# Kernel tuning notes

Hardware: AMD Instinct MI355X
Metric: run time of the kernel (lower is better)

Reference implementation:

```python
import jax, jax.numpy as jnp
import numpy as np

B, N, VD, QD, D, H, NG, P = 512, 36, 2048, 1024, 1024, 16, 20, 64
DH = D // H  # per-head dim = 64


def setup_inputs() -> dict:
    key = jax.random.key(0)
    ks = jax.random.split(key, 20)
    s = 0.02
    return {
        "visual": jax.random.normal(ks[0], (B, N, VD), jnp.float32),
        "pos_emb": jax.random.uniform(ks[1], (B, N, NG, P), jnp.float32),
        "question": jax.random.normal(ks[2], (B, QD), jnp.float32),
        # v2out: FC v_dim -> out_dim with ReLU
        "v2out_w": s * jax.random.normal(ks[3], (VD, D), jnp.float32),
        "v2out_b": jnp.zeros((D,), jnp.float32),
        # GAttNet self_weights: (out_dim+q_dim) -> out_dim, no activation
        "self_w": s * jax.random.normal(ks[4], (D + QD, D), jnp.float32),
        "self_b": jnp.zeros((D,), jnp.float32),
        # attention query/key projections (feat_dim -> feat_dim)
        "q_w": s * jax.random.normal(ks[5], (D, D), jnp.float32),
        "q_b": jnp.zeros((D,), jnp.float32),
        "k_w": s * jax.random.normal(ks[6], (D, D), jnp.float32),
        "k_b": jnp.zeros((D,), jnp.float32),
        # pair_pos_fc1: pos_emb_dim -> num_heads (fc_dim)
        "pos_w": s * jax.random.normal(ks[7], (P, H), jnp.float32),
        "pos_b": jnp.zeros((H,), jnp.float32),
        # label bias FC: label_num(=1) -> 1, with bias (label_bias=True)
        "bias_w": s * jax.random.normal(ks[8], (1, 1), jnp.float32),
        "bias_b": jnp.zeros((1,), jnp.float32),
        # grouped 1x1 conv linear_out_: per-head [feat_dim -> feat_dim/H]
        "out_w": s * jax.random.normal(ks[9], (H, D, DH), jnp.float32),
        "out_b": jnp.zeros((D,), jnp.float32),
    }


def reference(visual, pos_emb, question, v2out_w, v2out_b, self_w, self_b,
              q_w, q_b, k_w, k_b, pos_w, pos_b, bias_w, bias_b, out_w, out_b):
    b, n, _ = visual.shape
    ng = pos_emb.shape[2]

    # v2out projection (FCNet default ReLU)
    vis = jax.nn.relu(visual @ v2out_w + v2out_b)  # [B,N,D]

    # dense all-ones adjacency [B,N,N,1]; condensed over labels and sliced to nongt
    adj = jnp.ones((b, n, ng), vis.dtype)                       # sum over label dim
    label_bias = adj * bias_w[0, 0] + bias_b[0]                  # [B,N,NG]

    # --- single propagation step (num_steps=1) ---
    # concat_visual_question with mask
    row_mask = (jnp.sum(vis, axis=-1) != 0).astype(vis.dtype)    # [B,N]
    q_bcast = question[:, None, :] * row_mask[..., None]         # [B,N,QD]
    v_cat_q = jnp.concatenate([vis, q_bcast], axis=-1)           # [B,N,D+QD]

    # GAttNet: self loop features
    self_feat = v_cat_q @ self_w + self_b                        # [B,N,D]

    # GraphSelfAttentionLayer on self_feat
    ngf = self_feat[:, :ng]                                      # [B,NG,D]
    q = (self_feat @ q_w + q_b).reshape(b, n, H, DH)             # [B,N,H,DH]
    k = (ngf @ k_w + k_b).reshape(b, ng, H, DH)                  # [B,NG,H,DH]
    scale = np.float32(1.0 / np.sqrt(DH))
    aff = jnp.einsum('bnhd,bmhd->bnhm', q, k) * scale            # [B,N,H,NG]

    # relational position bias: relu -> clamp -> log
    pos_feat = jax.nn.relu(pos_emb @ pos_w + pos_b)              # [B,N,NG,H]
    aff = aff + jnp.transpose(jnp.log(jnp.maximum(pos_feat, 1e-6)), (0, 1, 3, 2))

    # adjacency mask + label bias
    aff = jnp.where(adj[:, :, None, :] > 0, aff, jnp.float32(-9e15))
    aff = aff + label_bias[:, :, None, :]

    attn = jax.nn.softmax(aff, axis=-1)                          # [B,N,H,NG]
    out_t = jnp.einsum('bnhm,bmf->bnhf', attn, ngf)              # [B,N,H,D]
    neighbor = jnp.einsum('bnhf,hfd->bnhd', out_t, out_w).reshape(b, n, D) + out_b

    imp_rel = jax.nn.relu(self_feat + neighbor)                  # GAttNet output

    # residual connection
    return vis + imp_rel
```

## Files before the change

### kernel.cpp

```cpp
#include <hip/hip_runtime.h>
#include <cstdint>

#define AS1 __attribute__((address_space(1)))
#define AS3 __attribute__((address_space(3)))

typedef __bf16 bf16x8 __attribute__((ext_vector_type(8)));
typedef float f32x4 __attribute__((ext_vector_type(4)));

__device__ __forceinline__ unsigned short f2bf(float f) {
  unsigned u = __float_as_uint(f);
  u += 0x7FFFu + ((u >> 16) & 1u);
  return (unsigned short)(u >> 16);
}
__device__ __forceinline__ float bf2f(unsigned short s) {
  return __uint_as_float(((unsigned)s) << 16);
}

__global__ void k_f32_to_bf16(const float* __restrict__ in,
                              unsigned short* __restrict__ out, long n8) {
  long i = (long)blockIdx.x * blockDim.x + threadIdx.x;
  if (i >= n8) return;
  const float4* p = (const float4*)in + i * 2;
  float4 a = p[0], b = p[1];
  uint4 o;
  o.x = (unsigned)f2bf(a.x) | ((unsigned)f2bf(a.y) << 16);
  o.y = (unsigned)f2bf(a.z) | ((unsigned)f2bf(a.w) << 16);
  o.z = (unsigned)f2bf(b.x) | ((unsigned)f2bf(b.y) << 16);
  o.w = (unsigned)f2bf(b.z) | ((unsigned)f2bf(b.w) << 16);
  *((uint4*)out + i) = o;
}

__global__ void k_transpose_bf16(const float* __restrict__ in,
                                 unsigned short* __restrict__ out, int R, int C) {
  __shared__ float tile[32][33];
  int c0 = blockIdx.x * 32, r0 = blockIdx.y * 32;
  int tx = threadIdx.x & 31, ty = threadIdx.x >> 5;
  #pragma unroll
  for (int i = ty; i < 32; i += 8) tile[i][tx] = in[(long)(r0 + i) * C + c0 + tx];
  __syncthreads();
  #pragma unroll
  for (int i = ty; i < 32; i += 8) out[(long)(c0 + i) * R + r0 + tx] = f2bf(tile[tx][i]);
}

__global__ void k_transpose_outw(const float* __restrict__ in,
                                 unsigned short* __restrict__ out) {
  __shared__ float tile[32][33];
  int d0 = blockIdx.x * 32, f0 = blockIdx.y * 32, h = blockIdx.z;
  int tx = threadIdx.x & 31, ty = threadIdx.x >> 5;
  #pragma unroll
  for (int i = ty; i < 32; i += 8)
    tile[i][tx] = in[((long)h * 1024 + f0 + i) * 64 + d0 + tx];
  __syncthreads();
  #pragma unroll
  for (int i = ty; i < 32; i += 8)
    out[((long)h * 64 + d0 + i) * 1024 + f0 + tx] = f2bf(tile[tx][i]);
}

enum { EPI_VIS = 0, EPI_QW, EPI_SELF, EPI_Q, EPI_K, EPI_KG };

template <int EPI>
__global__ __launch_bounds__(256) void k_gemm(
    const unsigned short* __restrict__ A, const unsigned short* __restrict__ Bt,
    int M, int K,
    const float* __restrict__ bias,
    const float* __restrict__ mask, const float* __restrict__ QW,
    float* __restrict__ outf, unsigned short* __restrict__ outb,
    unsigned short* __restrict__ ngf) {
  (void)M;
  __shared__ __align__(16) unsigned short As[128 * 64];
  __shared__ __align__(16) unsigned short Bs[128 * 64];
  const int t = threadIdx.x;
  const int l = t & 63, w = t >> 6;
  const int wm = w >> 1, wn = w & 1;
  const long bm0 = (long)blockIdx.y * 128, bn0 = (long)blockIdx.x * 128;

  f32x4 acc[4][4];
  #pragma unroll
  for (int i = 0; i < 4; ++i)
    #pragma unroll
    for (int j = 0; j < 4; ++j) acc[i][j] = (f32x4){0.f, 0.f, 0.f, 0.f};

  const int lrow = l & 15;
  const int lkbase = (l >> 4) * 8;

  for (int k0 = 0; k0 < K; k0 += 64) {
    #pragma unroll
    for (int i = 0; i < 4; ++i) {
      int c = i * 256 + t;
      int row = c >> 3, cc = (c & 7) << 3;
      const unsigned short* ga = A + (bm0 + row) * (long)K + k0 + cc;
      const unsigned short* gb = Bt + (bn0 + row) * (long)K + k0 + cc;
      int ldsoff = __builtin_amdgcn_readfirstlane((i * 256 + w * 64) * 8);
      __builtin_amdgcn_global_load_lds((AS1 void*)ga, (AS3 void*)(As + ldsoff), 16, 0, 0);
      __builtin_amdgcn_global_load_lds((AS1 void*)gb, (AS3 void*)(Bs + ldsoff), 16, 0, 0);
    }
    __syncthreads();
    #pragma unroll
    for (int kk = 0; kk < 2; ++kk) {
      bf16x8 af[4], bfr[4];
      const int lk = kk * 32 + lkbase;
      #pragma unroll
      for (int mf = 0; mf < 4; ++mf)
        af[mf] = *(const bf16x8*)(As + (wm * 64 + mf * 16 + lrow) * 64 + lk);
      #pragma unroll
      for (int nf = 0; nf < 4; ++nf)
        bfr[nf] = *(const bf16x8*)(Bs + (wn * 64 + nf * 16 + lrow) * 64 + lk);
      #pragma unroll
      for (int mf = 0; mf < 4; ++mf)
        #pragma unroll
        for (int nf = 0; nf < 4; ++nf)
          acc[mf][nf] = __builtin_amdgcn_mfma_f32_16x16x32_bf16(af[mf], bfr[nf],
                                                                acc[mf][nf], 0, 0, 0);
    }
    __syncthreads();
  }

  #pragma unroll
  for (int mf = 0; mf < 4; ++mf) {
    #pragma unroll
    for (int r = 0; r < 4; ++r) {
      long row = bm0 + wm * 64 + mf * 16 + ((l >> 4) << 2) + r;
      #pragma unroll
      for (int nf = 0; nf < 4; ++nf) {
        long col = bn0 + wn * 64 + nf * 16 + (l & 15);
        float x = acc[mf][nf][r];
        long idx = row * 1024 + col;
        if (EPI == EPI_VIS) {
          x += bias[col];
          x = fmaxf(x, 0.f);
          outf[idx] = x;
          outb[idx] = f2bf(x);
        } else if (EPI == EPI_QW) {
          outf[idx] = x;
        } else if (EPI == EPI_SELF) {
          int b = (int)(row / 36), n = (int)(row % 36);
          x += bias[col] + mask[row] * QW[(long)b * 1024 + col];
          outf[idx] = x;
          outb[idx] = f2bf(x);
          if (n < 20) ngf[((long)b * 20 + n) * 1024 + col] = f2bf(x);
        } else if (EPI == EPI_Q) {
          x += bias[col];
          outb[idx] = f2bf(x);
        } else if (EPI == EPI_K) {
          x += bias[col];
          outb[idx] = f2bf(x);
        } else {
          outb[idx] = f2bf(x);
        }
      }
    }
  }
}

__global__ void k_mask(const float* __restrict__ vis, float* __restrict__ mask) {
  int row = blockIdx.x * 4 + (threadIdx.x >> 6);
  int l = threadIdx.x & 63;
  const float4* vr = (const float4*)(vis + (long)row * 1024);
  float s = 0.f;
  #pragma unroll
  for (int i = 0; i < 4; ++i) {
    float4 v = vr[l + i * 64];
    s += v.x + v.y + v.z + v.w;
  }
  #pragma unroll
  for (int st = 1; st < 64; st <<= 1) s += __shfl_xor(s, st);
  if (l == 0) mask[row] = (s != 0.f) ? 1.f : 0.f;
}

__global__ __launch_bounds__(256) void k_poslogit(const float* __restrict__ pos_emb,
                                                  const float* __restrict__ pos_w,
                                                  const float* __restrict__ pos_b,
                                                  float* __restrict__ plog) {
  __shared__ float wsm[64 * 16];
  __shared__ float bsm[16];
  int t = threadIdx.x;
  for (int i = t; i < 1024; i += 256) wsm[i] = pos_w[i];
  if (t < 16) bsm[t] = pos_b[t];
  __syncthreads();
  long row = (long)blockIdx.x * 16 + (t >> 4);
  int h = t & 15;
  const float4* pr = (const float4*)(pos_emb + row * 64);
  float acc = bsm[h];
  #pragma unroll
  for (int i = 0; i < 16; ++i) {
    float4 v = pr[i];
    acc += v.x * wsm[(i * 4 + 0) * 16 + h];
    acc += v.y * wsm[(i * 4 + 1) * 16 + h];
    acc += v.z * wsm[(i * 4 + 2) * 16 + h];
    acc += v.w * wsm[(i * 4 + 3) * 16 + h];
  }
  acc = fmaxf(acc, 1e-6f);
  plog[row * 16 + h] = __logf(acc);
}

__global__ __launch_bounds__(1024) void k_attn(
    const unsigned short* __restrict__ qb, const unsigned short* __restrict__ kb,
    const unsigned short* __restrict__ kgb, const float* __restrict__ plog,
    const float* __restrict__ selff, const float* __restrict__ visf,
    const float* __restrict__ outbias, float* __restrict__ out) {
  int bn = blockIdx.x;
  int b = bn / 36;
  int h = threadIdx.x >> 6;
  int l = threadIdx.x & 63;
  long base = (long)bn * 1024 + h * 64 + l;
  float qv = bf2f(qb[base]);
  float aff[20];
  #pragma unroll
  for (int m = 0; m < 20; ++m) {
    float kv = bf2f(kb[((long)(b * 20 + m) << 10) + h * 64 + l]);
    float p = qv * kv;
    #pragma unroll
    for (int st = 1; st < 64; st <<= 1) p += __shfl_xor(p, st);
    aff[m] = p * 0.125f + plog[((long)(bn * 20 + m) << 4) + h];
  }
  float amax = aff[0];
  #pragma unroll
  for (int m = 1; m < 20; ++m) amax = fmaxf(amax, aff[m]);
  float s = 0.f;
  #pragma unroll
  for (int m = 0; m < 20; ++m) {
    aff[m] = __expf(aff[m] - amax);
    s += aff[m];
  }
  float inv = 1.f / s;
  float nb = 0.f;
  #pragma unroll
  for (int m = 0; m < 20; ++m)
    nb += aff[m] * bf2f(kgb[((long)(b * 20 + m) << 10) + h * 64 + l]);
  nb = nb * inv + outbias[h * 64 + l];
  float x = selff[base] + nb;
  out[base] = visf[base] + fmaxf(x, 0.f);
}

extern "C" void kernel_launch(void* const* d_in, const int* in_sizes, int n_in,
                              void* d_out, int out_size, void* d_ws, size_t ws_size,
                              hipStream_t stream) {
  (void)in_sizes; (void)n_in; (void)out_size; (void)ws_size;
  const float* visual   = (const float*)d_in[0];
  const float* pos_emb  = (const float*)d_in[1];
  const float* question = (const float*)d_in[2];
  const float* v2out_w  = (const float*)d_in[3];
  const float* v2out_b  = (const float*)d_in[4];
  const float* self_w   = (const float*)d_in[5];
  const float* self_b   = (const float*)d_in[6];
  const float* q_w      = (const float*)d_in[7];
  const float* q_b      = (const float*)d_in[8];
  const float* k_w      = (const float*)d_in[9];
  const float* k_b      = (const float*)d_in[10];
  const float* pos_w    = (const float*)d_in[11];
  const float* pos_b    = (const float*)d_in[12];
  const float* out_w    = (const float*)d_in[15];
  const float* out_b    = (const float*)d_in[16];
  float* out = (float*)d_out;

  char* ws = (char*)d_ws;
  size_t off = 0;
  auto alloc = [&](size_t bytes) -> void* {
    off = (off + 255) & ~(size_t)255;
    void* p = ws + off;
    off += bytes;
    return p;
  };

  unsigned short* visual_bf   = (unsigned short*)alloc(18432L * 2048 * 2);
  unsigned short* question_bf = (unsigned short*)alloc(512L * 1024 * 2);
  unsigned short* v2out_wt    = (unsigned short*)alloc(1024L * 2048 * 2);
  unsigned short* self_w1t    = (unsigned short*)alloc(1024L * 1024 * 2);
  unsigned short* self_w2t    = (unsigned short*)alloc(1024L * 1024 * 2);
  unsigned short* q_wt        = (unsigned short*)alloc(1024L * 1024 * 2);
  unsigned short* k_wt        = (unsigned short*)alloc(1024L * 1024 * 2);
  unsigned short* outw_bt     = (unsigned short*)alloc(1024L * 1024 * 2);
  float*          vis_f       = (float*)alloc(18432L * 1024 * 4);
  unsigned short* vis_bf      = (unsigned short*)alloc(18432L * 1024 * 2);
  float*          self_f      = (float*)alloc(18432L * 1024 * 4);
  unsigned short* self_bf     = (unsigned short*)alloc(18432L * 1024 * 2);
  unsigned short* ngf_bf      = (unsigned short*)alloc(10240L * 1024 * 2);
  unsigned short* q_bf        = (unsigned short*)alloc(18432L * 1024 * 2);
  unsigned short* k_bf        = (unsigned short*)alloc(10240L * 1024 * 2);
  unsigned short* kg_bf       = (unsigned short*)alloc(10240L * 1024 * 2);
  float*          plog        = (float*)alloc(368640L * 16 * 4);
  float*          QW          = (float*)alloc(512L * 1024 * 4);
  float*          maskp       = (float*)alloc(18432L * 4);

  k_f32_to_bf16<<<18432, 256, 0, stream>>>(visual, visual_bf, 18432L * 2048 / 8);
  k_f32_to_bf16<<<256, 256, 0, stream>>>(question, question_bf, 512L * 1024 / 8);
  k_transpose_bf16<<<dim3(32, 64), 256, 0, stream>>>(v2out_w, v2out_wt, 2048, 1024);
  k_transpose_bf16<<<dim3(32, 32), 256, 0, stream>>>(self_w, self_w1t, 1024, 1024);
  k_transpose_bf16<<<dim3(32, 32), 256, 0, stream>>>(self_w + 1024L * 1024, self_w2t, 1024, 1024);
  k_transpose_bf16<<<dim3(32, 32), 256, 0, stream>>>(q_w, q_wt, 1024, 1024);
  k_transpose_bf16<<<dim3(32, 32), 256, 0, stream>>>(k_w, k_wt, 1024, 1024);
  k_transpose_outw<<<dim3(2, 32, 16), 256, 0, stream>>>(out_w, outw_bt);

  k_gemm<EPI_VIS><<<dim3(8, 144), 256, 0, stream>>>(visual_bf, v2out_wt, 18432, 2048,
      v2out_b, nullptr, nullptr, vis_f, vis_bf, nullptr);
  k_mask<<<4608, 256, 0, stream>>>(vis_f, maskp);
  k_gemm<EPI_QW><<<dim3(8, 4), 256, 0, stream>>>(question_bf, self_w2t, 512, 1024,
      nullptr, nullptr, nullptr, QW, nullptr, nullptr);
  k_gemm<EPI_SELF><<<dim3(8, 144), 256, 0, stream>>>(vis_bf, self_w1t, 18432, 1024,
      self_b, maskp, QW, self_f, self_bf, ngf_bf);
  k_gemm<EPI_Q><<<dim3(8, 144), 256, 0, stream>>>(self_bf, q_wt, 18432, 1024,
      q_b, nullptr, nullptr, nullptr, q_bf, nullptr);
  k_gemm<EPI_K><<<dim3(8, 80), 256, 0, stream>>>(ngf_bf, k_wt, 10240, 1024,
      k_b, nullptr, nullptr, nullptr, k_bf, nullptr);
  k_gemm<EPI_KG><<<dim3(8, 80), 256, 0, stream>>>(ngf_bf, outw_bt, 10240, 1024,
      nullptr, nullptr, nullptr, nullptr, kg_bf, nullptr);
  k_poslogit<<<23040, 256, 0, stream>>>(pos_emb, pos_w, pos_b, plog);
  k_attn<<<18432, 1024, 0, stream>>>(q_bf, k_bf, kg_bf, plog, self_f, vis_f, out_b, out);
}
```

Baseline: 1.200 ms.

## Restructure attention kernel per batch with LDS-staged K/KG and bf16 residual inputs

The attention kernel now runs one block per batch (576 threads, one per (head, node)) and stages K and then KG into LDS with global_load_lds. Each thread computes its 20 affinities directly instead of doing a per-element shuffle reduction, and writes bf16 softmax weights to LDS for a vectorized aggregation pass. The fp32 copies of vis and self features are no longer written. The mask and the final residual read the bf16 buffers instead, which cuts global memory traffic. This trades fp32 precision in the residual and the attention weights for bandwidth, and it may lower occupancy because of the large LDS footprint.

Result: slower. 1.394 ms (+16.2%).

```diff
diff --git a/kernel.cpp b/kernel.cpp
--- a/kernel.cpp
+++ b/kernel.cpp
@@ -12,8 +12,14 @@
   u += 0x7FFFu + ((u >> 16) & 1u);
   return (unsigned short)(u >> 16);
 }
-__device__ __forceinline__ float bf2f(unsigned short s) {
-  return __uint_as_float(((unsigned)s) << 16);
+__device__ __forceinline__ float bflo(unsigned u) { return __uint_as_float(u << 16); }
+__device__ __forceinline__ float bfhi(unsigned u) { return __uint_as_float(u & 0xFFFF0000u); }
+
+__device__ __forceinline__ void unpack8(uint4 r, float* f) {
+  f[0] = bflo(r.x); f[1] = bfhi(r.x);
+  f[2] = bflo(r.y); f[3] = bfhi(r.y);
+  f[4] = bflo(r.z); f[5] = bfhi(r.z);
+  f[6] = bflo(r.w); f[7] = bfhi(r.w);
 }
 
 __global__ void k_f32_to_bf16(const float* __restrict__ in,
@@ -128,14 +134,12 @@
         if (EPI == EPI_VIS) {
           x += bias[col];
           x = fmaxf(x, 0.f);
-          outf[idx] = x;
           outb[idx] = f2bf(x);
         } else if (EPI == EPI_QW) {
           outf[idx] = x;
         } else if (EPI == EPI_SELF) {
           int b = (int)(row / 36), n = (int)(row % 36);
           x += bias[col] + mask[row] * QW[(long)b * 1024 + col];
-          outf[idx] = x;
           outb[idx] = f2bf(x);
           if (n < 20) ngf[((long)b * 20 + n) * 1024 + col] = f2bf(x);
         } else if (EPI == EPI_Q) {
@@ -152,19 +156,19 @@
   }
 }
 
-__global__ void k_mask(const float* __restrict__ vis, float* __restrict__ mask) {
+__global__ void k_mask(const unsigned short* __restrict__ vis, float* __restrict__ mask) {
   int row = blockIdx.x * 4 + (threadIdx.x >> 6);
   int l = threadIdx.x & 63;
-  const float4* vr = (const float4*)(vis + (long)row * 1024);
-  float s = 0.f;
-  #pragma unroll
-  for (int i = 0; i < 4; ++i) {
-    float4 v = vr[l + i * 64];
-    s += v.x + v.y + v.z + v.w;
-  }
-  #pragma unroll
-  for (int st = 1; st < 64; st <<= 1) s += __shfl_xor(s, st);
-  if (l == 0) mask[row] = (s != 0.f) ? 1.f : 0.f;
+  const uint4* vr = (const uint4*)(vis + (long)row * 1024);
+  unsigned s = 0;
+  #pragma unroll
+  for (int i = 0; i < 2; ++i) {
+    uint4 v = vr[l + i * 64];
+    s |= v.x | v.y | v.z | v.w;
+  }
+  #pragma unroll
+  for (int st = 1; st < 64; st <<= 1) s |= __shfl_xor(s, st);
+  if (l == 0) mask[row] = (s != 0) ? 1.f : 0.f;
 }
 
 __global__ __launch_bounds__(256) void k_poslogit(const float* __restrict__ pos_emb,
@@ -193,43 +197,132 @@
   plog[row * 16 + h] = __logf(acc);
 }
 
-__global__ __launch_bounds__(1024) void k_attn(
+__global__ __launch_bounds__(576, 5) void k_attn(
     const unsigned short* __restrict__ qb, const unsigned short* __restrict__ kb,
     const unsigned short* __restrict__ kgb, const float* __restrict__ plog,
-    const float* __restrict__ selff, const float* __restrict__ visf,
+    const unsigned short* __restrict__ selfb, const unsigned short* __restrict__ visb,
     const float* __restrict__ outbias, float* __restrict__ out) {
-  int bn = blockIdx.x;
-  int b = bn / 36;
-  int h = threadIdx.x >> 6;
-  int l = threadIdx.x & 63;
-  long base = (long)bn * 1024 + h * 64 + l;
-  float qv = bf2f(qb[base]);
+  __shared__ __align__(16) unsigned short lds[32000];
+  const int t = threadIdx.x;
+  const int b = blockIdx.x;
+  const int w = t >> 6;
+
+  if (w < 8) {
+    const unsigned short* srcK = kb + (long)b * 20480;
+    #pragma unroll
+    for (int k = 0; k < 5; ++k) {
+      int chunk = k * 512 + t;
+      int ldsoff = __builtin_amdgcn_readfirstlane((k * 512 + w * 64) * 16);
+      __builtin_amdgcn_global_load_lds((AS1 void*)(srcK + chunk * 8),
+                                       (AS3 void*)((char*)lds + ldsoff), 16, 0, 0);
+    }
+  }
+
+  const int h = t / 36, n = t - h * 36;
+  const long qrow = (long)b * 36 + n;
+  const unsigned short* qp = qb + (qrow << 10) + h * 64;
+
   float aff[20];
   #pragma unroll
-  for (int m = 0; m < 20; ++m) {
-    float kv = bf2f(kb[((long)(b * 20 + m) << 10) + h * 64 + l]);
-    float p = qv * kv;
-    #pragma unroll
-    for (int st = 1; st < 64; st <<= 1) p += __shfl_xor(p, st);
-    aff[m] = p * 0.125f + plog[((long)(bn * 20 + m) << 4) + h];
-  }
-  float amax = aff[0];
-  #pragma unroll
-  for (int m = 1; m < 20; ++m) amax = fmaxf(amax, aff[m]);
-  float s = 0.f;
-  #pragma unroll
-  for (int m = 0; m < 20; ++m) {
-    aff[m] = __expf(aff[m] - amax);
-    s += aff[m];
-  }
-  float inv = 1.f / s;
-  float nb = 0.f;
-  #pragma unroll
-  for (int m = 0; m < 20; ++m)
-    nb += aff[m] * bf2f(kgb[((long)(b * 20 + m) << 10) + h * 64 + l]);
-  nb = nb * inv + outbias[h * 64 + l];
-  float x = selff[base] + nb;
-  out[base] = visf[base] + fmaxf(x, 0.f);
+  for (int m = 0; m < 20; ++m) aff[m] = 0.f;
+
+  __syncthreads();
+
+  const int kbase = h * 64;
+  #pragma unroll
+  for (int d0 = 0; d0 < 8; ++d0) {
+    uint4 qraw = *(const uint4*)(qp + d0 * 8);
+    float qf[8];
+    unpack8(qraw, qf);
+    #pragma unroll
+    for (int m = 0; m < 20; ++m) {
+      uint4 kraw = *(const uint4*)(lds + m * 1024 + kbase + d0 * 8);
+      float kf[8];
+      unpack8(kraw, kf);
+      #pragma unroll
+      for (int i = 0; i < 8; ++i) aff[m] += qf[i] * kf[i];
+    }
+  }
+
+  __syncthreads();
+
+  if (w < 8) {
+    const unsigned short* srcG = kgb + (long)b * 20480;
+    #pragma unroll
+    for (int k = 0; k < 5; ++k) {
+      int chunk = k * 512 + t;
+      int ldsoff = __builtin_amdgcn_readfirstlane((k * 512 + w * 64) * 16);
+      __builtin_amdgcn_global_load_lds((AS1 void*)(srcG + chunk * 8),
+                                       (AS3 void*)((char*)lds + ldsoff), 16, 0, 0);
+    }
+  }
+
+  {
+    const float* pl = plog + ((qrow * 20) << 4) + h;
+    #pragma unroll
+    for (int m = 0; m < 20; ++m) aff[m] = aff[m] * 0.125f + pl[m * 16];
+    float amax = aff[0];
+    #pragma unroll
+    for (int m = 1; m < 20; ++m) amax = fmaxf(amax, aff[m]);
+    float s = 0.f;
+    #pragma unroll
+    for (int m = 0; m < 20; ++m) {
+      aff[m] = __expf(aff[m] - amax);
+      s += aff[m];
+    }
+    float inv = 1.f / s;
+    unsigned short* ap = lds + 20480 + t * 20;
+    #pragma unroll
+    for (int m = 0; m < 20; m += 2) {
+      unsigned lo = f2bf(aff[m] * inv), hi = f2bf(aff[m + 1] * inv);
+      *(unsigned*)(ap + m) = lo | (hi << 16);
+    }
+  }
+
+  __syncthreads();
+
+  const long obase = (long)b * 36864;
+  #pragma unroll
+  for (int j = 0; j < 16; ++j) {
+    int f = (j * 576 + t) << 2;
+    int n2 = f >> 10;
+    int hd = f & 1023;
+    const unsigned short* ap = lds + 20480 + ((hd >> 6) * 36 + n2) * 20;
+    unsigned av[10];
+    #pragma unroll
+    for (int i = 0; i < 5; ++i) {
+      uint2 v = *(const uint2*)(ap + i * 4);
+      av[2 * i] = v.x;
+      av[2 * i + 1] = v.y;
+    }
+    f32x4 acc = (f32x4){0.f, 0.f, 0.f, 0.f};
+    #pragma unroll
+    for (int m = 0; m < 20; m += 2) {
+      unsigned apair = av[m >> 1];
+      float a0 = bflo(apair), a1 = bfhi(apair);
+      const unsigned short* g0 = lds + m * 1024 + hd;
+      uint2 r0 = *(const uint2*)g0;
+      uint2 r1 = *(const uint2*)(g0 + 1024);
+      acc[0] += a0 * bflo(r0.x);
+      acc[1] += a0 * bfhi(r0.x);
+      acc[2] += a0 * bflo(r0.y);
+      acc[3] += a0 * bfhi(r0.y);
+      acc[0] += a1 * bflo(r1.x);
+      acc[1] += a1 * bfhi(r1.x);
+      acc[2] += a1 * bflo(r1.y);
+      acc[3] += a1 * bfhi(r1.y);
+    }
+    long gidx = obase + f;
+    uint2 sv = *(const uint2*)(selfb + gidx);
+    uint2 vv = *(const uint2*)(visb + gidx);
+    float4 bi = *(const float4*)(outbias + hd);
+    float4 o;
+    o.x = bflo(vv.x) + fmaxf(bflo(sv.x) + acc[0] + bi.x, 0.f);
+    o.y = bfhi(vv.x) + fmaxf(bfhi(sv.x) + acc[1] + bi.y, 0.f);
+    o.z = bflo(vv.y) + fmaxf(bflo(sv.y) + acc[2] + bi.z, 0.f);
+    o.w = bfhi(vv.y) + fmaxf(bfhi(sv.y) + acc[3] + bi.w, 0.f);
+    *(float4*)(out + gidx) = o;
+  }
 }
 
 extern "C" void kernel_launch(void* const* d_in, const int* in_sizes, int n_in,
@@ -270,9 +363,7 @@
   unsigned short* q_wt        = (unsigned short*)alloc(1024L * 1024 * 2);
   unsigned short* k_wt        = (unsigned short*)alloc(1024L * 1024 * 2);
   unsigned short* outw_bt     = (unsigned short*)alloc(1024L * 1024 * 2);
-  float*          vis_f       = (float*)alloc(18432L * 1024 * 4);
   unsigned short* vis_bf      = (unsigned short*)alloc(18432L * 1024 * 2);
-  float*          self_f      = (float*)alloc(18432L * 1024 * 4);
   unsigned short* self_bf     = (unsigned short*)alloc(18432L * 1024 * 2);
   unsigned short* ngf_bf      = (unsigned short*)alloc(10240L * 1024 * 2);
   unsigned short* q_bf        = (unsigned short*)alloc(18432L * 1024 * 2);
@@ -292,12 +383,12 @@
   k_transpose_outw<<<dim3(2, 32, 16), 256, 0, stream>>>(out_w, outw_bt);
 
   k_gemm<EPI_VIS><<<dim3(8, 144), 256, 0, stream>>>(visual_bf, v2out_wt, 18432, 2048,
-      v2out_b, nullptr, nullptr, vis_f, vis_bf, nullptr);
-  k_mask<<<4608, 256, 0, stream>>>(vis_f, maskp);
+      v2out_b, nullptr, nullptr, nullptr, vis_bf, nullptr);
+  k_mask<<<4608, 256, 0, stream>>>(vis_bf, maskp);
   k_gemm<EPI_QW><<<dim3(8, 4), 256, 0, stream>>>(question_bf, self_w2t, 512, 1024,
       nullptr, nullptr, nullptr, QW, nullptr, nullptr);
   k_gemm<EPI_SELF><<<dim3(8, 144), 256, 0, stream>>>(vis_bf, self_w1t, 18432, 1024,
-      self_b, maskp, QW, self_f, self_bf, ngf_bf);
+      self_b, maskp, QW, nullptr, self_bf, ngf_bf);
   k_gemm<EPI_Q><<<dim3(8, 144), 256, 0, stream>>>(self_bf, q_wt, 18432, 1024,
       q_b, nullptr, nullptr, nullptr, q_bf, nullptr);
   k_gemm<EPI_K><<<dim3(8, 80), 256, 0, stream>>>(ngf_bf, k_wt, 10240, 1024,
@@ -305,5 +396,5 @@
   k_gemm<EPI_KG><<<dim3(8, 80), 256, 0, stream>>>(ngf_bf, outw_bt, 10240, 1024,
       nullptr, nullptr, nullptr, nullptr, kg_bf, nullptr);
   k_poslogit<<<23040, 256, 0, stream>>>(pos_emb, pos_w, pos_b, plog);
-  k_attn<<<18432, 1024, 0, stream>>>(q_bf, k_bf, kg_bf, plog, self_f, vis_f, out_b, out);
-}
+  k_attn<<<512, 576, 0, stream>>>(q_bf, k_bf, kg_bf, plog, self_bf, vis_bf, out_b, out);
+}
```
